# Kernel optimization log

Measured on AMD Instinct MI355X. Metric: run time of the kernel, lower is better.

Reference implementation:

```python
import jax, jax.numpy as jnp
import numpy as np

PS = (3, 5, 9)
RMAP = (3, 2, 1)
CHUNK = 1024
TAU = 1.0
RADIUS = 2
DILATION = 2


def _mind_kernels():
    six = np.array([[0, 1, 1], [1, 1, 0], [1, 0, 1], [1, 1, 2], [2, 1, 1], [1, 2, 1]])
    dist = ((six[:, None, :] - six[None, :, :]) ** 2).sum(-1)  # squared dists, [6,6]
    x, y = np.meshgrid(np.arange(6), np.arange(6), indexing='ij')
    mask = (x > y).reshape(-1) & (dist == 2).reshape(-1)
    idx1 = np.repeat(six[:, None, :], 6, 1).reshape(-1, 3)[mask]
    idx2 = np.repeat(six[None, :, :], 6, 0).reshape(-1, 3)[mask]
    m1 = np.zeros((12, 1, 3, 3, 3), np.float32)
    m2 = np.zeros((12, 1, 3, 3, 3), np.float32)
    m1[np.arange(12), 0, idx1[:, 0], idx1[:, 1], idx1[:, 2]] = 1.0
    m2[np.arange(12), 0, idx2[:, 0], idx2[:, 1], idx2[:, 2]] = 1.0
    return jnp.asarray(m1), jnp.asarray(m2)


def mindssc(img):
    m1, m2 = _mind_kernels()
    dn = ('NCDHW', 'OIDHW', 'NCDHW')
    d = DILATION
    xp = jnp.pad(img, [(0, 0), (0, 0), (d, d), (d, d), (d, d)], mode='edge')
    c1 = jax.lax.conv_general_dilated(xp, m1, (1, 1, 1), 'VALID', rhs_dilation=(d, d, d), dimension_numbers=dn)
    c2 = jax.lax.conv_general_dilated(xp, m2, (1, 1, 1), 'VALID', rhs_dilation=(d, d, d), dimension_numbers=dn)
    diff2 = (c1 - c2) ** 2  # [B,12,D,H,W]
    r = RADIUS
    dp = jnp.pad(diff2, [(0, 0), (0, 0), (r, r), (r, r), (r, r)], mode='edge')
    k = 2 * r + 1
    ssd = jax.lax.reduce_window(dp, 0.0, jax.lax.add, (1, 1, k, k, k), (1, 1, 1, 1, 1), 'VALID') / float(k ** 3)
    mind = ssd - ssd.min(axis=1, keepdims=True)
    mv = mind.mean(axis=1, keepdims=True)
    mm = mv.mean()
    mv = jnp.clip(mv, mm * 0.001, mm * 1000.0)
    mind = jnp.exp(-mind / mv)
    order = jnp.array([6, 8, 1, 11, 2, 10, 0, 7, 9, 4, 5, 3])
    return mind[:, order]


def unfold(x, p):
    B, C, D, H, W = x.shape  # D,H,W divisible by p for the chosen shapes
    Nz, Ny, Nx = D // p, H // p, W // p
    patches = x.reshape(B, C, Nz, p, Ny, p, Nx, p)
    patches = patches.transpose(0, 2, 4, 6, 1, 3, 5, 7).reshape(B, Nz * Ny * Nx, C * p ** 3)
    return patches, (Nz, Ny, Nx)


def local_loss(pa, pb, grid, R):
    # L2-normalize patch descriptors (F.normalize eps=1e-12)
    pa = pa / jnp.maximum(jnp.linalg.norm(pa, axis=-1, keepdims=True), 1e-12)
    pb = pb / jnp.maximum(jnp.linalg.norm(pb, axis=-1, keepdims=True), 1e-12)
    B, N, C = pa.shape
    nC = -(-N // CHUNK)
    Np = nC * CHUNK
    pa_p = jnp.pad(pa, ((0, 0), (0, Np - N), (0, 0)))
    grid_p = jnp.pad(grid, ((0, Np - N), (0, 0)))
    idx_p = jnp.arange(Np, dtype=jnp.int32)
    pa_ch = pa_p.reshape(B, nC, CHUNK, C).transpose(1, 0, 2, 3)   # [nC,B,chunk,C]
    grid_ch = grid_p.reshape(nC, CHUNK, 3)
    idx_ch = idx_p.reshape(nC, CHUNK)

    def body(tot, xs):
        pac, gc, ic = xs
        sim = jnp.einsum('bnc,bmc->bnm', pac, pb)                 # [B,chunk,N]
        keep = jnp.all(jnp.abs(gc[:, None, :] - grid[None, :, :]) <= R, axis=-1)  # [chunk,N]
        sim = jnp.where(keep[None], sim, -1e9) / TAU
        lse = jax.nn.logsumexp(sim, axis=-1)                      # [B,chunk]
        col = jnp.clip(ic, 0, N - 1)
        aligned = jnp.take_along_axis(sim, col[None, :, None], axis=2)[..., 0]
        valid = (ic < N).astype(sim.dtype)
        tot = tot + ((lse - aligned) * valid[None]).sum()
        return tot, None

    tot, _ = jax.lax.scan(body, jnp.float32(0.0), (pa_ch, grid_ch, idx_ch))
    return tot / (B * N)


def setup_inputs() -> dict:
    key = jax.random.key(0)
    k1, k2 = jax.random.split(key)
    fixed = jax.random.normal(k1, (2, 1, 90, 90, 90), dtype=jnp.float32)
    moving = jax.random.normal(k2, (2, 1, 90, 90, 90), dtype=jnp.float32)
    scale_w = jnp.full((3,), 1.0 / 3.0, dtype=jnp.float32)  # default scale_weights
    return {'fixed': fixed, 'moving': moving, 'scale_w': scale_w}


def reference(fixed, moving, scale_w):
    mind_f = mindssc(fixed)
    mind_m = mindssc(moving)
    w = jax.nn.softmax(scale_w, axis=0)
    total = jnp.float32(0.0)
    for i, (p, R) in enumerate(zip(PS, RMAP)):
        pf, (Nz, Ny, Nx) = unfold(mind_f, p)
        pm, _ = unfold(mind_m, p)
        gz, gy, gx = jnp.meshgrid(jnp.arange(Nz), jnp.arange(Ny), jnp.arange(Nx), indexing='ij')
        grid = jnp.stack([gz, gy, gx], -1).reshape(-1, 3).astype(jnp.int32)
        total = total + w[i] * local_loss(pf, pm, grid, R)
    return total
```

## Files before the change

kernel.cpp:

```cpp
#include <hip/hip_runtime.h>
#include <hip/hip_bf16.h>
#include <math.h>

#define VOL 729000
#define SL  8100
#define RW  90

typedef __attribute__((ext_vector_type(8))) short s8v;
typedef __attribute__((ext_vector_type(4))) float f32x4;

__device__ __constant__ int c_o1[12][3] = {
  {0,0,-2},{0,-2,0},{0,-2,0},{0,0,2},{0,0,2},{2,0,0},{2,0,0},{2,0,0},{0,2,0},{0,2,0},{0,2,0},{0,2,0}
};
__device__ __constant__ int c_o2[12][3] = {
  {-2,0,0},{-2,0,0},{0,0,-2},{-2,0,0},{0,-2,0},{0,0,-2},{0,-2,0},{0,0,2},{-2,0,0},{0,0,-2},{0,0,2},{2,0,0}
};

__device__ __forceinline__ int clampi(int v, int lo, int hi){ return v<lo?lo:(v>hi?hi:v); }

typedef __attribute__((address_space(3))) uint lds_uint;
typedef __attribute__((address_space(1))) uint glb_uint;
__device__ __forceinline__ void gl_lds16(const ushort* g, ushort* l) {
  __builtin_amdgcn_global_load_lds((const glb_uint*)g, (lds_uint*)l, 16, 0, 0);
}
__device__ __forceinline__ float bf2f(uint u) { return __uint_as_float(u << 16); }
__device__ __forceinline__ ushort f2bf(float f) {
  __hip_bfloat16 h = __float2bfloat16(f);
  return *(ushort*)&h;
}

__global__ __launch_bounds__(256) void zy_kernel(const float* __restrict__ img,
                                                 float* __restrict__ out) {
  __shared__ float zb[8100];
  int nwg = gridDim.x;
  int q = nwg >> 3, r8 = nwg & 7;
  int xcd = blockIdx.x & 7, sidx = blockIdx.x >> 3;
  int lid = (xcd < r8 ? xcd*(q+1) : r8*(q+1) + (xcd - r8)*q) + sidx;
  int z = lid % 90; int bc = lid / 90; int t = bc % 12; int b = bc / 12;
  const float* im = img + (size_t)b*VOL;
  int o1z=c_o1[t][0], o1y=c_o1[t][1], o1x=c_o1[t][2];
  int o2z=c_o2[t][0], o2y=c_o2[t][1], o2x=c_o2[t][2];
  int tid = threadIdx.x;
  int z1a[5], z2a[5];
  #pragma unroll
  for (int d=0; d<5; ++d) {
    int zz = clampi(z+d-2,0,89);
    z1a[d] = clampi(zz+o1z,0,89);
    z2a[d] = clampi(zz+o2z,0,89);
  }
  for (int i = tid; i < 8100; i += 256) {
    int y = i/90, x = i - (i/90)*90;
    int y1 = clampi(y+o1y,0,89), x1 = clampi(x+o1x,0,89);
    int y2 = clampi(y+o2y,0,89), x2 = clampi(x+o2x,0,89);
    float s = 0.f;
    #pragma unroll
    for (int d=0; d<5; ++d) {
      float dv = im[z1a[d]*SL + y1*RW + x1] - im[z2a[d]*SL + y2*RW + x2];
      s += dv*dv;
    }
    zb[i] = s;
  }
  __syncthreads();
  float* ob = out + (size_t)bc*VOL + (size_t)z*SL;
  for (int i = tid; i < 8100; i += 256) {
    int y = i/90; int x = i - y*90;
    float s = 0.f;
    #pragma unroll
    for (int d=-2; d<=2; ++d) { int yc = clampi(y+d,0,89); s += zb[yc*90 + x]; }
    ob[i] = s;
  }
}

__global__ void boxxmin_kernel(const float* __restrict__ in, ushort* __restrict__ outPre,
                               float* __restrict__ mvsum) {
  __shared__ float red;
  if (threadIdx.x == 0) red = 0.f;
  __syncthreads();
  int idx = blockIdx.x*256 + threadIdx.x;
  float mv = 0.f;
  if (idx < 2*VOL) {
    int b = idx / VOL; int vox = idx % VOL;
    int z = vox / SL; int r = vox % SL; int y = r / RW; int x = r % RW;
    const float* base = in + (size_t)b*12*VOL + (size_t)z*SL + (size_t)y*RW;
    float s[12]; float mn = 3.4e38f;
    #pragma unroll
    for (int c=0;c<12;++c) {
      const float* pc = base + (size_t)c*VOL;
      float t = 0.f;
      #pragma unroll
      for (int d=-2;d<=2;++d) { int xc = clampi(x+d,0,89); t += pc[xc]; }
      t *= (1.0f/125.0f);
      s[c] = t; mn = fminf(mn, t);
    }
    ushort* ob = outPre + (size_t)b*12*VOL + vox;
    #pragma unroll
    for (int c=0;c<12;++c) { float pre = s[c]-mn; ob[(size_t)c*VOL] = f2bf(pre); mv += pre; }
    mv *= (1.0f/12.0f);
  }
  #pragma unroll
  for (int o=32;o;o>>=1) mv += __shfl_xor(mv, o);
  if ((threadIdx.x & 63)==0 && mv != 0.f) atomicAdd(&red, mv);
  __syncthreads();
  if (threadIdx.x==0) atomicAdd(mvsum, red);
}

__global__ void finalize_kernel(const ushort* __restrict__ pre, ushort* __restrict__ out,
                                const float* __restrict__ mvsum) {
  int idx = blockIdx.x*256 + threadIdx.x;
  if (idx >= 2*VOL) return;
  int b = idx / VOL; int vox = idx % VOL;
  const ushort* base = pre + (size_t)b*12*VOL + vox;
  ushort* ob = out + (size_t)b*12*VOL + vox;
  float s[12]; float mv = 0.f;
  #pragma unroll
  for (int c=0;c<12;++c) { s[c] = bf2f(base[(size_t)c*VOL]); mv += s[c]; }
  mv *= (1.0f/12.0f);
  float mm = *mvsum * (1.0f/1458000.0f);
  float mvc = fminf(fmaxf(mv, mm*0.001f), mm*1000.0f);
  float inv = 1.0f / mvc;
  #pragma unroll
  for (int c=0;c<12;++c) ob[(size_t)c*VOL] = f2bf(__expf(-s[c]*inv));
}

template<int P, int CCH>
__global__ __launch_bounds__(256) void packn_kernel(const ushort* __restrict__ Ybf,
                                                    ushort* __restrict__ pk,
                                                    float* __restrict__ inv) {
  constexpr int NG=90/P, N=NG*NG*NG, C=12*P*P*P;
  constexpr int P2=P*P, P3=P*P*P;
  constexpr int ROWS = CCH*P2;
  constexpr int HALF = CCH*P3/2;
  __shared__ uint slabU[ROWS*48];
  int blk = blockIdx.x;
  int gy = blk % NG; int t1 = blk / NG; int gz = t1 % NG; int b = t1 / NG;
  int tid = threadIdx.x;
  size_t dbase = (size_t)b*N + ((size_t)gz*NG + gy)*NG;
  size_t obase = dbase * C;
  for (int c0 = 0; c0 < 12; c0 += CCH) {
    if (c0) __syncthreads();
    for (int i = tid; i < ROWS*45; i += 256) {
      int r = i/45, xu = i - r*45;
      int c = c0 + r/P2; int rr = r % P2; int dz = rr/P, dy = rr - dz*P;
      const ushort* src = Ybf + ((size_t)(b*12 + c)*VOL + (size_t)(gz*P+dz)*SL + (size_t)(gy*P+dy)*RW);
      slabU[r*48 + xu] = *(const uint*)(src + 2*xu);
    }
    __syncthreads();
    const ushort* slab = (const ushort*)slabU;
    for (int i = tid; i < NG*HALF; i += 256) {
      int d = i/HALF, j2 = i - d*HALF;
      int k = 2*j2;
      int cc = k/P3; int rem = k - cc*P3;
      int dz = rem/P2; int r2 = rem - dz*P2; int dy = r2/P; int dx = r2 - dy*P;
      uint lo = slab[((cc*P + dz)*P + dy)*96 + d*P + dx];
      int k1 = k+1;
      int cc1 = k1/P3; int rem1 = k1 - cc1*P3;
      int dz1 = rem1/P2; int r21 = rem1 - dz1*P2; int dy1 = r21/P; int dx1 = r21 - dy1*P;
      uint hi = slab[((cc1*P + dz1)*P + dy1)*96 + d*P + dx1];
      *(uint*)(pk + obase + (size_t)d*C + c0*P3 + k) = lo | (hi << 16);
    }
  }
  __syncthreads();
  int wv2 = tid >> 6, lane2 = tid & 63;
  for (int d = wv2; d < NG; d += 4) {
    const uint* p = (const uint*)(pk + obase + (size_t)d*C);
    float ss = 0.f;
    for (int i = lane2; i < C/2; i += 64) {
      uint u = p[i];
      float a = bf2f(u & 0xffffu), b2 = bf2f(u >> 16);
      ss += a*a + b2*b2;
    }
    #pragma unroll
    for (int o=32;o;o>>=1) ss += __shfl_xor(ss, o);
    if (lane2==0) inv[dbase + d] = 1.0f / fmaxf(sqrtf(ss), 1e-12f);
  }
}

union FragU { s8v s; uint u[4]; };
__device__ __forceinline__ s8v ldfrag_m(const ushort* p, bool v0, bool v1) {
  FragU f;
  if (v0) { uint2 a = *(const uint2*)p;     f.u[0]=a.x; f.u[1]=a.y; } else { f.u[0]=0; f.u[1]=0; }
  if (v1) { uint2 b = *(const uint2*)(p+4); f.u[2]=b.x; f.u[3]=b.y; } else { f.u[2]=0; f.u[3]=0; }
  return f.s;
}

template<int P, int R, int JM, int XT, int TPB, int KB, int NCHMAX, int CPW>
__global__ __launch_bounds__(TPB) void loss_kernel(
    const ushort* __restrict__ pkF, const ushort* __restrict__ pkM,
    const float* __restrict__ invF, const float* __restrict__ invM,
    float* __restrict__ sumG, float* __restrict__ alnG) {
  constexpr int NG=90/P, N=NG*NG*NG, C=12*P*P*P;
  constexpr int NW=TPB/64;
  constexpr int AT=JM*XT;
  constexpr int KS4=(C & ~31)/32;
  constexpr int NPH=(KS4+KB-1)/KB;
  constexpr int NROWS=AT*16;
  constexpr int NJG=(2*R+1+JM-1)/JM;
  constexpr int SLOTS=(AT+NCHMAX)*KB;
  constexpr int TOTS=((SLOTS+NW-1)/NW)*NW;
  constexpr int TCNT=TOTS/NW;
  static_assert(XT*16 >= NG, "x tiles cover line");
  static_assert(CPW*NW >= NCHMAX, "chunk coverage");
  static_assert(KS4 % KB == 0, "no K tail in phases");
  __shared__ float sumS[NROWS];
  __shared__ float invAS[NROWS];
  __shared__ __align__(16) ushort bP[2][SLOTS*512];

  int nwg = gridDim.x;
  int q = nwg >> 3, r8 = nwg & 7;
  int xcd = blockIdx.x & 7, sidx = blockIdx.x >> 3;
  int lid = (xcd < r8 ? xcd*(q+1) : r8*(q+1) + (xcd - r8)*q) + sidx;
  int jg = lid % NJG; int t1 = lid / NJG;
  int gy = t1 % NG; t1 /= NG;
  int mz = t1 % NG; int b = t1 / NG;
  int gz0 = mz - R + jg*JM;
  bool any = false;
  #pragma unroll
  for (int g=0; g<JM; ++g)
    any |= (jg*JM+g <= 2*R) && ((unsigned)(gz0+g) < (unsigned)NG);
  if (!any) return;

  int tid = threadIdx.x; int lane = tid & 63; int wv = tid >> 6;
  int col = lane & 15, grp = lane >> 4;
  const int ko = grp*8;

  const ushort* aRow[AT];
  #pragma unroll
  for (int at=0; at<AT; ++at) {
    int gzi = at/XT, xt = at%XT;
    int gzc = clampi(gz0+gzi, 0, NG-1);
    int xd = xt*16 + col; if (xd > NG-1) xd = NG-1;
    aRow[at] = pkF + ((size_t)b*N + ((size_t)gzc*NG + gy)*NG + xd) * C;
  }
  for (int i = tid; i < NROWS; i += TPB) {
    sumS[i] = 0.f;
    int at = i >> 4, sub = i & 15;
    int gzi = at/XT, x = (at%XT)*16 + sub;
    bool lvr = (jg*JM+gzi <= 2*R) && ((unsigned)(gz0+gzi) < (unsigned)NG) && (x < NG);
    invAS[i] = lvr ? invF[(size_t)b*N + ((size_t)(gz0+gzi)*NG + gy)*NG + x] : 0.f;
  }

  int y0 = max(gy-R,0), y1 = min(gy+R,NG-1);
  int wy = y1-y0+1;
  int Ms = wy*NG;
  int nch = (Ms+15)>>4;
  const ushort* sliceM = pkM + ((size_t)b*N + ((size_t)mz*NG + y0)*NG) * C;
  const float* invMsl  = invM + (size_t)b*N + ((size_t)mz*NG + y0)*NG;

  const ushort* srcB[TCNT];
  int dstO[TCNT];
  #pragma unroll
  for (int k = 0; k < TCNT; ++k) {
    int i2 = wv + k*NW;
    int ii = i2 < SLOTS ? i2 : SLOTS-1;
    int slot = ii / KB, s = ii - slot*KB;
    const ushort* sb;
    if (slot < AT) {
      sb = aRow[slot];
    } else {
      int c = slot - AT; if (c > nch-1) c = nch-1;
      int di = c*16 + col; if (di > Ms-1) di = Ms-1;
      sb = sliceM + (size_t)di*C;
    }
    srcB[k] = sb + s*32 + ko;
    dstO[k] = ii*512;
  }
  auto stage = [&](int ph, ushort* dst) {
    #pragma unroll
    for (int k = 0; k < TCNT; ++k)
      gl_lds16(srcB[k] + ph*(KB*32), dst + dstO[k]);
  };

  stage(0, bP[0]);
  __syncthreads();

  f32x4 acc[CPW][AT];
  #pragma unroll
  for (int ci=0;ci<CPW;++ci)
    #pragma unroll
    for (int at=0;at<AT;++at) acc[ci][at] = (f32x4){0.f,0.f,0.f,0.f};

  for (int ph = 0; ph < NPH; ++ph) {
    if (ph+1 < NPH) {
      stage(ph+1, bP[(ph+1)&1]);
      asm volatile("s_waitcnt vmcnt(%0)" :: "i"(TCNT) : "memory");
    } else {
      asm volatile("s_waitcnt vmcnt(0)" ::: "memory");
    }
    __builtin_amdgcn_sched_barrier(0);
    asm volatile("s_barrier" ::: "memory");
    const ushort* buf = bP[ph&1];
    __builtin_amdgcn_s_setprio(1);
    #pragma unroll
    for (int s = 0; s < KB; ++s) {
      s8v bf[CPW];
      #pragma unroll
      for (int ci=0; ci<CPW; ++ci) {
        int c = wv + ci*NW;
        if (c < nch) bf[ci] = *(const s8v*)(buf + ((AT + c)*KB + s)*512 + lane*8);
      }
      #pragma unroll
      for (int at=0; at<AT; ++at) {
        s8v af = *(const s8v*)(buf + (at*KB + s)*512 + lane*8);
        #pragma unroll
        for (int ci=0; ci<CPW; ++ci) {
          int c = wv + ci*NW;
          if (c < nch)
            acc[ci][at] = __builtin_amdgcn_mfma_f32_16x16x32_bf16(af, bf[ci], acc[ci][at], 0,0,0);
        }
      }
    }
    __builtin_amdgcn_s_setprio(0);
    asm volatile("s_barrier" ::: "memory");
  }

  s8v aftA[AT]; bool tv0=false, tv1=false;
  if constexpr ((C & 31) != 0) {
    int kg = (C & ~31) + ko;
    tv0 = (kg+4 <= C); tv1 = (kg+8 <= C);
    #pragma unroll
    for (int at=0;at<AT;++at) aftA[at] = ldfrag_m(aRow[at] + (C & ~31) + ko, tv0, tv1);
  }

  float sumE[AT][4];
  #pragma unroll
  for (int at=0;at<AT;++at) { sumE[at][0]=0.f; sumE[at][1]=0.f; sumE[at][2]=0.f; sumE[at][3]=0.f; }

  #pragma unroll
  for (int ci=0; ci<CPW; ++ci) {
    int c = wv + ci*NW;
    if (c < nch) {
      int mu = c*16 + col; bool vm = mu < Ms;
      int mus = vm ? mu : 0;
      if constexpr ((C & 31) != 0) {
        s8v bft = ldfrag_m(sliceM + (size_t)mus*C + (C & ~31) + ko, tv0, tv1);
        #pragma unroll
        for (int at=0;at<AT;++at)
          acc[ci][at] = __builtin_amdgcn_mfma_f32_16x16x32_bf16(aftA[at], bft, acc[ci][at], 0,0,0);
      }
      float invBm = invMsl[mus];
      int myq = mus/NG; int my = y0 + myq; int mx = mus - myq*NG;
      #pragma unroll
      for (int at=0; at<AT; ++at) {
        int gzi = at/XT;
        bool lv = (jg*JM+gzi <= 2*R) && ((unsigned)(gz0+gzi) < (unsigned)NG);
        bool mzEq = lv && (gz0+gzi == mz);
        #pragma unroll
        for (int jj=0;jj<4;++jj) {
          int x = (at%XT)*16 + grp*4 + jj;
          int row = at*16 + grp*4 + jj;
          float sim = acc[ci][at][jj] * invAS[row] * invBm;
          bool ok = vm && lv && (x < NG) && (mx - x <= R) && (x - mx <= R);
          if (ok) {
            sumE[at][jj] += __expf(sim);
            if (mzEq && my==gy && mx==x)
              alnG[(size_t)b*N + ((size_t)(gz0+gzi)*NG + gy)*NG + x] = sim;
          }
        }
      }
    }
  }

  #pragma unroll
  for (int at=0;at<AT;++at) {
    #pragma unroll
    for (int jj=0;jj<4;++jj) {
      float v = sumE[at][jj];
      v += __shfl_xor(v,1); v += __shfl_xor(v,2); v += __shfl_xor(v,4); v += __shfl_xor(v,8);
      if (col==0 && v != 0.f) atomicAdd(&sumS[at*16 + grp*4 + jj], v);
    }
  }
  __syncthreads();
  for (int i = tid; i < NROWS; i += TPB) {
    int at = i >> 4, sub = i & 15;
    int gzi = at/XT, x = (at%XT)*16 + sub;
    bool lvr = (jg*JM+gzi <= 2*R) && ((unsigned)(gz0+gzi) < (unsigned)NG) && (x < NG);
    float v = sumS[i];
    if (lvr && v != 0.f)
      atomicAdd(&sumG[(size_t)b*N + ((size_t)(gz0+gzi)*NG + gy)*NG + x], v);
  }
}

__global__ void epilogue_kernel(const float* __restrict__ sumG, const float* __restrict__ alnG,
                                const float* __restrict__ sw, float* __restrict__ out) {
  constexpr int N3 = 54000, N5 = 11664, N9 = 2000;
  constexpr int TOT = N3 + N5 + N9;
  __shared__ float wred[4];
  int idx = blockIdx.x*256 + threadIdx.x;
  float w0 = sw[0], w1 = sw[1], w2 = sw[2];
  float mx = fmaxf(w0, fmaxf(w1, w2));
  float e0 = __expf(w0-mx), e1 = __expf(w1-mx), e2 = __expf(w2-mx);
  float ise = 1.0f/(e0+e1+e2);
  float c = 0.f;
  if (idx < TOT) {
    float coef;
    if (idx < N3)            coef = e0*ise/(float)N3;
    else if (idx < N3+N5)    coef = e1*ise/(float)N5;
    else                     coef = e2*ise/(float)N9;
    c = (__logf(sumG[idx]) - alnG[idx]) * coef;
  }
  #pragma unroll
  for (int o=32;o;o>>=1) c += __shfl_xor(c, o);
  if ((threadIdx.x & 63)==0) wred[threadIdx.x>>6] = c;
  __syncthreads();
  if (threadIdx.x==0) {
    float s = wred[0]+wred[1]+wred[2]+wred[3];
    if (s != 0.f) atomicAdd(out, s);
  }
}

static inline int cdiv(long long a, int b) { return (int)((a + b - 1) / b); }

template<int P, int R, int JM, int XT, int TPB, int KB, int NCHMAX, int CPW, int CCH>
static void run_scale(const ushort* Yf, const ushort* Ym, ushort* pkF, ushort* pkM,
                      float* invPF, float* invPM, float* sumG, float* alnG, hipStream_t s) {
  constexpr int NG=90/P, N=NG*NG*NG, C=12*P*P*P;
  constexpr int NJG=(2*R+1+JM-1)/JM;
  packn_kernel<P,CCH><<<2*NG*NG, 256, 0, s>>>(Yf, pkF, invPF);
  packn_kernel<P,CCH><<<2*NG*NG, 256, 0, s>>>(Ym, pkM, invPM);
  loss_kernel<P,R,JM,XT,TPB,KB,NCHMAX,CPW><<<2*NG*NG*NJG, TPB, 0, s>>>(
      pkF, pkM, invPF, invPM, sumG, alnG);
}

extern "C" void kernel_launch(void* const* d_in, const int* in_sizes, int n_in,
                              void* d_out, int out_size, void* d_ws, size_t ws_size,
                              hipStream_t stream) {
  const float* fixedI  = (const float*)d_in[0];
  const float* movingI = (const float*)d_in[1];
  const float* scale_w = (const float*)d_in[2];
  float* out = (float*)d_out;

  uint8_t* w = (uint8_t*)d_ws;
  float*  smallb = (float*)w;
  float*  sumG  = (float*)(w + 4096);
  float*  alnG  = sumG + 67664;
  float*  invPF = alnG + 67664;
  float*  invPM = invPF + 67664;
  uint8_t* big = w + (2u<<20);
  ushort* PK   = (ushort*)big;
  ushort* preB = PK;
  float*  Azy  = (float*)(big + 69984000);
  ushort* pkF  = PK;
  ushort* pkM  = PK + 17496000;
  ushort* Ybf_f = (ushort*)(big + 2*69984000ull);
  ushort* Ybf_m = Ybf_f + 17496000;

  hipMemsetAsync(w, 0, 4096 + 67664*4, stream);
  hipMemsetAsync(d_out, 0, sizeof(float), stream);

  const int gV = cdiv(1458000, 256);

  zy_kernel<<<2160,256,0,stream>>>(fixedI, Azy);
  boxxmin_kernel<<<gV,256,0,stream>>>(Azy, preB, smallb+0);
  finalize_kernel<<<gV,256,0,stream>>>(preB, Ybf_f, smallb+0);

  zy_kernel<<<2160,256,0,stream>>>(movingI, Azy);
  boxxmin_kernel<<<gV,256,0,stream>>>(Azy, preB, smallb+1);
  finalize_kernel<<<gV,256,0,stream>>>(preB, Ybf_m, smallb+1);

  run_scale<3,3,2,2,512,1,14,2,12>(Ybf_f, Ybf_m, pkF, pkM, invPF,         invPM,         sumG,         alnG,         stream);
  run_scale<5,2,3,2,384,1, 6,1, 6>(Ybf_f, Ybf_m, pkF, pkM, invPF + 54000, invPM + 54000, sumG + 54000, alnG + 54000, stream);
  run_scale<9,1,1,1,128,7, 2,1, 2>(Ybf_f, Ybf_m, pkF, pkM, invPF + 65664, invPM + 65664, sumG + 65664, alnG + 65664, stream);

  epilogue_kernel<<<cdiv(67664,256),256,0,stream>>>(sumG, alnG, scale_w, out);
}
```

Baseline: 1.016 ms.

## Batch fixed and moving preprocessing, store zy intermediate as bf16, split norm kernel

The zy, box/min, finalize and pack kernels now each handle the fixed and moving volumes in a single launch instead of two, which halves the number of launches and doubles the grid per launch. The zy intermediate is stored in bf16 instead of fp32, halving its write and read traffic in the next pass at some cost in precision. The per-patch L2-norm computation moves out of the pack kernel into a separate one-wave-per-patch kernel, which gives it more parallelism but costs an extra pass over the packed data.

```diff
diff --git a/kernel.cpp b/kernel.cpp
--- a/kernel.cpp
+++ b/kernel.cpp
@@ -29,15 +29,16 @@
   return *(ushort*)&h;
 }
 
-__global__ __launch_bounds__(256) void zy_kernel(const float* __restrict__ img,
-                                                 float* __restrict__ out) {
+__global__ __launch_bounds__(256) void zy_kernel(const float* __restrict__ imgF,
+                                                 const float* __restrict__ imgM,
+                                                 ushort* __restrict__ out) {
   __shared__ float zb[8100];
   int nwg = gridDim.x;
   int q = nwg >> 3, r8 = nwg & 7;
   int xcd = blockIdx.x & 7, sidx = blockIdx.x >> 3;
   int lid = (xcd < r8 ? xcd*(q+1) : r8*(q+1) + (xcd - r8)*q) + sidx;
-  int z = lid % 90; int bc = lid / 90; int t = bc % 12; int b = bc / 12;
-  const float* im = img + (size_t)b*VOL;
+  int z = lid % 90; int bc = lid / 90; int t = bc % 12; int bq = bc / 12;
+  const float* im = (bq < 2 ? imgF : imgM) + (size_t)(bq & 1)*VOL;
   int o1z=c_o1[t][0], o1y=c_o1[t][1], o1x=c_o1[t][2];
   int o2z=c_o2[t][0], o2y=c_o2[t][1], o2x=c_o2[t][2];
   int tid = threadIdx.x;
@@ -61,38 +62,41 @@
     zb[i] = s;
   }
   __syncthreads();
-  float* ob = out + (size_t)bc*VOL + (size_t)z*SL;
+  ushort* ob = out + (size_t)bc*VOL + (size_t)z*SL;
   for (int i = tid; i < 8100; i += 256) {
     int y = i/90; int x = i - y*90;
     float s = 0.f;
     #pragma unroll
     for (int d=-2; d<=2; ++d) { int yc = clampi(y+d,0,89); s += zb[yc*90 + x]; }
-    ob[i] = s;
-  }
-}
-
-__global__ void boxxmin_kernel(const float* __restrict__ in, ushort* __restrict__ outPre,
-                               float* __restrict__ mvsum) {
+    ob[i] = f2bf(s);
+  }
+}
+
+__global__ void boxxmin_kernel(const ushort* __restrict__ in, ushort* __restrict__ outPre,
+                               float* __restrict__ mvsum, int gV) {
   __shared__ float red;
   if (threadIdx.x == 0) red = 0.f;
   __syncthreads();
-  int idx = blockIdx.x*256 + threadIdx.x;
+  int blk = blockIdx.x;
+  int img = blk >= gV;
+  int idx = (img ? blk - gV : blk)*256 + threadIdx.x;
   float mv = 0.f;
   if (idx < 2*VOL) {
     int b = idx / VOL; int vox = idx % VOL;
+    int bq = img*2 + b;
     int z = vox / SL; int r = vox % SL; int y = r / RW; int x = r % RW;
-    const float* base = in + (size_t)b*12*VOL + (size_t)z*SL + (size_t)y*RW;
+    const ushort* base = in + (size_t)bq*12*VOL + (size_t)z*SL + (size_t)y*RW;
     float s[12]; float mn = 3.4e38f;
     #pragma unroll
     for (int c=0;c<12;++c) {
-      const float* pc = base + (size_t)c*VOL;
+      const ushort* pc = base + (size_t)c*VOL;
       float t = 0.f;
       #pragma unroll
-      for (int d=-2;d<=2;++d) { int xc = clampi(x+d,0,89); t += pc[xc]; }
+      for (int d=-2;d<=2;++d) { int xc = clampi(x+d,0,89); t += bf2f(pc[xc]); }
       t *= (1.0f/125.0f);
       s[c] = t; mn = fminf(mn, t);
     }
-    ushort* ob = outPre + (size_t)b*12*VOL + vox;
+    ushort* ob = outPre + (size_t)bq*12*VOL + vox;
     #pragma unroll
     for (int c=0;c<12;++c) { float pre = s[c]-mn; ob[(size_t)c*VOL] = f2bf(pre); mv += pre; }
     mv *= (1.0f/12.0f);
@@ -101,21 +105,24 @@
   for (int o=32;o;o>>=1) mv += __shfl_xor(mv, o);
   if ((threadIdx.x & 63)==0 && mv != 0.f) atomicAdd(&red, mv);
   __syncthreads();
-  if (threadIdx.x==0) atomicAdd(mvsum, red);
+  if (threadIdx.x==0) atomicAdd(mvsum + img, red);
 }
 
 __global__ void finalize_kernel(const ushort* __restrict__ pre, ushort* __restrict__ out,
-                                const float* __restrict__ mvsum) {
-  int idx = blockIdx.x*256 + threadIdx.x;
+                                const float* __restrict__ mvsum, int gV) {
+  int blk = blockIdx.x;
+  int img = blk >= gV;
+  int idx = (img ? blk - gV : blk)*256 + threadIdx.x;
   if (idx >= 2*VOL) return;
   int b = idx / VOL; int vox = idx % VOL;
-  const ushort* base = pre + (size_t)b*12*VOL + vox;
-  ushort* ob = out + (size_t)b*12*VOL + vox;
+  int bq = img*2 + b;
+  const ushort* base = pre + (size_t)bq*12*VOL + vox;
+  ushort* ob = out + (size_t)bq*12*VOL + vox;
   float s[12]; float mv = 0.f;
   #pragma unroll
   for (int c=0;c<12;++c) { s[c] = bf2f(base[(size_t)c*VOL]); mv += s[c]; }
   mv *= (1.0f/12.0f);
-  float mm = *mvsum * (1.0f/1458000.0f);
+  float mm = mvsum[img] * (1.0f/1458000.0f);
   float mvc = fminf(fmaxf(mv, mm*0.001f), mm*1000.0f);
   float inv = 1.0f / mvc;
   #pragma unroll
@@ -124,24 +131,26 @@
 
 template<int P, int CCH>
 __global__ __launch_bounds__(256) void packn_kernel(const ushort* __restrict__ Ybf,
-                                                    ushort* __restrict__ pk,
-                                                    float* __restrict__ inv) {
+                                                    ushort* __restrict__ pk) {
   constexpr int NG=90/P, N=NG*NG*NG, C=12*P*P*P;
   constexpr int P2=P*P, P3=P*P*P;
   constexpr int ROWS = CCH*P2;
   constexpr int HALF = CCH*P3/2;
+  constexpr int NGG = 2*NG*NG;
   __shared__ uint slabU[ROWS*48];
-  int blk = blockIdx.x;
+  int blk0 = blockIdx.x;
+  int img = blk0 >= NGG;
+  int blk = img ? blk0 - NGG : blk0;
   int gy = blk % NG; int t1 = blk / NG; int gz = t1 % NG; int b = t1 / NG;
+  int bq = img*2 + b;
   int tid = threadIdx.x;
-  size_t dbase = (size_t)b*N + ((size_t)gz*NG + gy)*NG;
-  size_t obase = dbase * C;
+  size_t obase = ((size_t)img*2*N + (size_t)b*N + ((size_t)gz*NG + gy)*NG) * C;
   for (int c0 = 0; c0 < 12; c0 += CCH) {
     if (c0) __syncthreads();
     for (int i = tid; i < ROWS*45; i += 256) {
       int r = i/45, xu = i - r*45;
       int c = c0 + r/P2; int rr = r % P2; int dz = rr/P, dy = rr - dz*P;
-      const ushort* src = Ybf + ((size_t)(b*12 + c)*VOL + (size_t)(gz*P+dz)*SL + (size_t)(gy*P+dy)*RW);
+      const ushort* src = Ybf + ((size_t)(bq*12 + c)*VOL + (size_t)(gz*P+dz)*SL + (size_t)(gy*P+dy)*RW);
       slabU[r*48 + xu] = *(const uint*)(src + 2*xu);
     }
     __syncthreads();
@@ -159,20 +168,25 @@
       *(uint*)(pk + obase + (size_t)d*C + c0*P3 + k) = lo | (hi << 16);
     }
   }
-  __syncthreads();
-  int wv2 = tid >> 6, lane2 = tid & 63;
-  for (int d = wv2; d < NG; d += 4) {
-    const uint* p = (const uint*)(pk + obase + (size_t)d*C);
-    float ss = 0.f;
-    for (int i = lane2; i < C/2; i += 64) {
-      uint u = p[i];
-      float a = bf2f(u & 0xffffu), b2 = bf2f(u >> 16);
-      ss += a*a + b2*b2;
-    }
-    #pragma unroll
-    for (int o=32;o;o>>=1) ss += __shfl_xor(ss, o);
-    if (lane2==0) inv[dbase + d] = 1.0f / fmaxf(sqrtf(ss), 1e-12f);
-  }
+}
+
+template<int C>
+__global__ __launch_bounds__(64) void normk(const ushort* __restrict__ pkBase,
+                                            float* __restrict__ invF,
+                                            float* __restrict__ invM, int twoN) {
+  int d0 = blockIdx.x; int lane = threadIdx.x;
+  int img = d0 >= twoN;
+  int di = img ? d0 - twoN : d0;
+  const uint* p = (const uint*)(pkBase + (size_t)img*17496000 + (size_t)di*C);
+  float ss = 0.f;
+  for (int i = lane; i < C/2; i += 64) {
+    uint u = p[i];
+    float a = bf2f(u & 0xffffu), bb = bf2f(u >> 16);
+    ss += a*a + bb*bb;
+  }
+  #pragma unroll
+  for (int o=32;o;o>>=1) ss += __shfl_xor(ss, o);
+  if (lane==0) (img ? invM : invF)[di] = 1.0f / fmaxf(sqrtf(ss), 1e-12f);
 }
 
 union FragU { s8v s; uint u[4]; };
@@ -411,12 +425,12 @@
 static inline int cdiv(long long a, int b) { return (int)((a + b - 1) / b); }
 
 template<int P, int R, int JM, int XT, int TPB, int KB, int NCHMAX, int CPW, int CCH>
-static void run_scale(const ushort* Yf, const ushort* Ym, ushort* pkF, ushort* pkM,
+static void run_scale(const ushort* Ybf, ushort* pkF, ushort* pkM,
                       float* invPF, float* invPM, float* sumG, float* alnG, hipStream_t s) {
   constexpr int NG=90/P, N=NG*NG*NG, C=12*P*P*P;
   constexpr int NJG=(2*R+1+JM-1)/JM;
-  packn_kernel<P,CCH><<<2*NG*NG, 256, 0, s>>>(Yf, pkF, invPF);
-  packn_kernel<P,CCH><<<2*NG*NG, 256, 0, s>>>(Ym, pkM, invPM);
+  packn_kernel<P,CCH><<<2*2*NG*NG, 256, 0, s>>>(Ybf, pkF);
+  normk<C><<<4*N, 64, 0, s>>>(pkF, invPF, invPM, 2*N);
   loss_kernel<P,R,JM,XT,TPB,KB,NCHMAX,CPW><<<2*NG*NG*NJG, TPB, 0, s>>>(
       pkF, pkM, invPF, invPM, sumG, alnG);
 }
@@ -436,30 +450,25 @@
   float*  invPF = alnG + 67664;
   float*  invPM = invPF + 67664;
   uint8_t* big = w + (2u<<20);
-  ushort* PK   = (ushort*)big;
-  ushort* preB = PK;
-  float*  Azy  = (float*)(big + 69984000);
-  ushort* pkF  = PK;
-  ushort* pkM  = PK + 17496000;
-  ushort* Ybf_f = (ushort*)(big + 2*69984000ull);
-  ushort* Ybf_m = Ybf_f + 17496000;
+  ushort* PK    = (ushort*)big;
+  ushort* preB  = PK;
+  ushort* Azy   = (ushort*)(big + 69984000);
+  ushort* pkF   = PK;
+  ushort* pkM   = PK + 17496000;
+  ushort* Ybf   = (ushort*)(big + 2*69984000ull);
 
   hipMemsetAsync(w, 0, 4096 + 67664*4, stream);
   hipMemsetAsync(d_out, 0, sizeof(float), stream);
 
   const int gV = cdiv(1458000, 256);
 
-  zy_kernel<<<2160,256,0,stream>>>(fixedI, Azy);
-  boxxmin_kernel<<<gV,256,0,stream>>>(Azy, preB, smallb+0);
-  finalize_kernel<<<gV,256,0,stream>>>(preB, Ybf_f, smallb+0);
-
-  zy_kernel<<<2160,256,0,stream>>>(movingI, Azy);
-  boxxmin_kernel<<<gV,256,0,stream>>>(Azy, preB, smallb+1);
-  finalize_kernel<<<gV,256,0,stream>>>(preB, Ybf_m, smallb+1);
-
-  run_scale<3,3,2,2,512,1,14,2,12>(Ybf_f, Ybf_m, pkF, pkM, invPF,         invPM,         sumG,         alnG,         stream);
-  run_scale<5,2,3,2,384,1, 6,1, 6>(Ybf_f, Ybf_m, pkF, pkM, invPF + 54000, invPM + 54000, sumG + 54000, alnG + 54000, stream);
-  run_scale<9,1,1,1,128,7, 2,1, 2>(Ybf_f, Ybf_m, pkF, pkM, invPF + 65664, invPM + 65664, sumG + 65664, alnG + 65664, stream);
+  zy_kernel<<<4320,256,0,stream>>>(fixedI, movingI, Azy);
+  boxxmin_kernel<<<2*gV,256,0,stream>>>(Azy, preB, smallb, gV);
+  finalize_kernel<<<2*gV,256,0,stream>>>(preB, Ybf, smallb, gV);
+
+  run_scale<3,3,2,2,512,1,14,2,12>(Ybf, pkF, pkM, invPF,         invPM,         sumG,         alnG,         stream);
+  run_scale<5,2,3,2,384,1, 6,1, 6>(Ybf, pkF, pkM, invPF + 54000, invPM + 54000, sumG + 54000, alnG + 54000, stream);
+  run_scale<9,1,1,1,128,7, 2,1, 2>(Ybf, pkF, pkM, invPF + 65664, invPM + 65664, sumG + 65664, alnG + 65664, stream);
 
   epilogue_kernel<<<cdiv(67664,256),256,0,stream>>>(sumG, alnG, scale_w, out);
 }
```

Measured after the change: 828.9 us. -18.5%, faster.
